# Performance work log

Hardware: AMD Instinct MI355X
Metric: run time of the kernel (lower is better)

Reference implementation:

```python
import jax, jax.numpy as jnp
import numpy as np

B, T, C = 4, 2048, 1024
H = 16
D = C // H  # 64


def setup_inputs() -> dict:
    key = jax.random.key(0)
    ks = jax.random.split(key, 5)
    scale = 0.02
    x = jax.random.normal(ks[0], (B, T, C), dtype=jnp.float32)
    # Linear weights stored in [in, out] layout (equivalent to torch W.T)
    W_qkv = jax.random.normal(ks[1], (C, 3 * C), dtype=jnp.float32) * scale
    b_qkv = jax.random.normal(ks[2], (3 * C,), dtype=jnp.float32) * scale
    W_out = jax.random.normal(ks[3], (C, C), dtype=jnp.float32) * scale
    b_out = jax.random.normal(ks[4], (C,), dtype=jnp.float32) * scale
    return {"x": x, "W_qkv": W_qkv, "b_qkv": b_qkv, "W_out": W_out, "b_out": b_out}


def reference(x, W_qkv, b_qkv, W_out, b_out):
    Bx, Tx, Cx = x.shape
    qkv = x @ W_qkv + b_qkv                      # [B,T,3C]
    qkv = qkv.reshape(Bx, Tx, 3, H, D)
    q = jnp.transpose(qkv[:, :, 0], (0, 2, 1, 3))  # [B,H,T,D]
    k = jnp.transpose(qkv[:, :, 1], (0, 2, 1, 3))
    v = jnp.transpose(qkv[:, :, 2], (0, 2, 1, 3))
    scores = jnp.einsum('bhqd,bhkd->bhqk', q, k) / jnp.sqrt(jnp.float32(D))
    causal = jnp.tril(jnp.ones((Tx, Tx), dtype=bool))  # keep lower triangle
    scores = jnp.where(causal, scores, jnp.float32(-jnp.inf))
    w = jax.nn.softmax(scores, axis=-1)           # dropout p=0.0 (eval)
    out = jnp.einsum('bhqk,bhkd->bhqd', w, v)     # [B,H,T,D]
    out = jnp.transpose(out, (0, 2, 1, 3)).reshape(Bx, Tx, Cx)
    return out @ W_out + b_out
```

## Files before the change

### kernel.cpp

```cpp
#include <hip/hip_runtime.h>

typedef _Float16 f16;
typedef _Float16 f16x4 __attribute__((ext_vector_type(4)));
typedef _Float16 f16x8 __attribute__((ext_vector_type(8)));
typedef float    f32x4 __attribute__((ext_vector_type(4)));

#define B_ 4
#define T_ 2048
#define C_ 1024
#define H_ 16
#define D_ 64

__device__ __forceinline__ void gload_lds16(const f16* g, f16* l) {
  __builtin_amdgcn_global_load_lds(
      (const __attribute__((address_space(1))) unsigned int*)g,
      (__attribute__((address_space(3))) unsigned int*)l, 16, 0, 0);
}

__global__ void cvt_kernel(const float* __restrict__ in, f16* __restrict__ out, int n4) {
  int i = blockIdx.x * blockDim.x + threadIdx.x;
  int stride = gridDim.x * blockDim.x;
  for (; i < n4; i += stride) {
    float4 v = ((const float4*)in)[i];
    f16x4 h = { (f16)v.x, (f16)v.y, (f16)v.z, (f16)v.w };
    ((f16x4*)out)[i] = h;
  }
}

__global__ void transpose_cvt_kernel(const float* __restrict__ W, f16* __restrict__ Wt,
                                     int K, int N) {
  __shared__ f16 tile[32][33];
  int bx = blockIdx.x, by = blockIdx.y;
  int tx = threadIdx.x & 31, ty = threadIdx.x >> 5;
  #pragma unroll
  for (int i = ty; i < 32; i += 8)
    tile[i][tx] = (f16)W[(size_t)(by * 32 + i) * N + bx * 32 + tx];
  __syncthreads();
  #pragma unroll
  for (int i = ty; i < 32; i += 8)
    Wt[(size_t)(bx * 32 + i) * K + by * 32 + tx] = tile[tx][i];
}

template <int EPI>
__global__ __launch_bounds__(256, 3)
void gemm_kernel(const f16* __restrict__ A, const f16* __restrict__ Bt,
                 const float* __restrict__ bias, float* __restrict__ outF,
                 f16* __restrict__ q, f16* __restrict__ kk, f16* __restrict__ vt,
                 int M, int N, int K) {
  __shared__ __align__(16) f16 As[3][128 * 32];
  __shared__ __align__(16) f16 Bs[3][128 * 32];
  const int nbn = N >> 7;
  const int bid = blockIdx.x;
  const int bm = bid / nbn, bn = bid % nbn;
  const int m0 = bm << 7, n0 = bn << 7;
  const int tid = threadIdx.x;
  const int lane = tid & 63, wid = tid >> 6;
  const int wr = wid >> 1, wc = wid & 1;

  f32x4 acc[4][4] = {};

  const int srow = lane >> 2;
  const int scol = (((lane & 3) ^ ((lane >> 2) & 3)) << 3);
  const f16* Abase = A + (size_t)(m0 + srow) * K + scol;
  const f16* Bbase = Bt + (size_t)(n0 + srow) * K + scol;

  auto stage = [&](int buf, int kt) {
    const int c0 = wid * 2;
    #pragma unroll
    for (int c = c0; c < c0 + 2; ++c) {
      gload_lds16(Abase + (size_t)c * 16 * K + kt * 32, &As[buf][c * 512]);
      gload_lds16(Bbase + (size_t)c * 16 * K + kt * 32, &Bs[buf][c * 512]);
    }
  };

  const int g = lane >> 4;
  const int rr = lane & 15;
  const int swz = (g ^ (rr & 3)) << 4;

  auto compute = [&](int buf) {
    f16x8 af[4], bf[4];
    #pragma unroll
    for (int t = 0; t < 4; ++t) {
      af[t] = *(const f16x8*)((const char*)&As[buf][0] + (wr * 64 + t * 16 + rr) * 64 + swz);
      bf[t] = *(const f16x8*)((const char*)&Bs[buf][0] + (wc * 64 + t * 16 + rr) * 64 + swz);
    }
    __builtin_amdgcn_s_setprio(1);
    #pragma unroll
    for (int i = 0; i < 4; ++i)
      #pragma unroll
      for (int j = 0; j < 4; ++j)
        acc[i][j] = __builtin_amdgcn_mfma_f32_16x16x32_f16(af[i], bf[j], acc[i][j], 0, 0, 0);
    __builtin_amdgcn_s_setprio(0);
  };

  const int nk = K >> 5;
  int bcur = 0, bnext = 1, bnn = 2;
  stage(0, 0);
  stage(1, 1);
  asm volatile("s_waitcnt vmcnt(4)" ::: "memory");
  __builtin_amdgcn_s_barrier();
  __builtin_amdgcn_sched_barrier(0);
  for (int t = 0; t < nk; ++t) {
    if (t + 2 < nk) stage(bnn, t + 2);
    compute(bcur);
    if (t + 1 < nk) {
      if (t + 2 < nk) asm volatile("s_waitcnt vmcnt(4)" ::: "memory");
      else            asm volatile("s_waitcnt vmcnt(0)" ::: "memory");
      __builtin_amdgcn_s_barrier();
      __builtin_amdgcn_sched_barrier(0);
    }
    const int tmp = bcur; bcur = bnext; bnext = bnn; bnn = tmp;
  }

  const int col = lane & 15;
  const int row4 = (lane >> 4) << 2;
  #pragma unroll
  for (int i = 0; i < 4; ++i) {
    #pragma unroll
    for (int j = 0; j < 4; ++j) {
      const int n = n0 + wc * 64 + j * 16 + col;
      const float bn_ = bias[n];
      #pragma unroll
      for (int r = 0; r < 4; ++r) {
        const int m = m0 + wr * 64 + i * 16 + row4 + r;
        const float v = acc[i][j][r] + bn_;
        if (EPI == 1) {
          outF[(size_t)m * N + n] = v;
        } else {
          const int which = n >> 10;
          const int cc = n & 1023;
          const int h = cc >> 6, d = cc & 63;
          const int b = m >> 11, t = m & 2047;
          const size_t bh = (size_t)b * 16 + h;
          const f16 hv = (f16)v;
          if (which == 0)      q [(bh * T_ + t) * D_ + d] = hv;
          else if (which == 1) kk[(bh * T_ + t) * D_ + d] = hv;
          else                 vt[(bh * D_ + d) * T_ + t] = hv;
        }
      }
    }
  }
}

__global__ __launch_bounds__(256, 2)
void attn_kernel(const f16* __restrict__ Q, const f16* __restrict__ Kg,
                 const f16* __restrict__ Vt, f16* __restrict__ Aout) {
  __shared__ __align__(16) f16 Ks[4][64 * 64];
  __shared__ __align__(16) f16 Vs[4][64 * 64];
  __shared__ __align__(16) f16 Pt[4][32 * 64];

  const int bid = blockIdx.x;
  const int wgid = (bid & 7) * 64 + (bid >> 3);
  const int bh = wgid >> 3;
  const int pr = wgid & 7;
  const int lane = threadIdx.x & 63, w = threadIdx.x >> 6;
  const int col = lane & 15;
  const int g = lane >> 4;
  const int ko = g << 3;

  const f16* Qp = Q + (size_t)bh * T_ * D_;
  const f16* Kp = Kg + (size_t)bh * T_ * D_;
  const f16* Vp = Vt + (size_t)bh * D_ * T_;

  const int sr = lane >> 3;
  const int sc = ((lane & 7) ^ (sr & 7)) << 3;

  auto stage = [&](int buf, int kb) {
    #pragma unroll
    for (int c2 = 0; c2 < 2; ++c2) {
      const int c = (w << 1) + c2;
      gload_lds16(Kp + (size_t)(kb + (c << 3) + sr) * D_ + sc, &Ks[buf][c * 512]);
      gload_lds16(Vp + (size_t)((c << 3) + sr) * T_ + kb + sc, &Vs[buf][c * 512]);
    }
  };
  auto ldsK = [&](int buf, int krow, int d0) -> f16x8 {
    const int off = krow * 128 + ((d0 << 1) ^ ((krow & 7) << 4));
    return *(const f16x8*)((const char*)&Ks[buf][0] + off);
  };
  auto ldsV = [&](int buf, int drow, int k0) -> f16x8 {
    const int off = drow * 128 + ((k0 << 1) ^ ((drow & 7) << 4));
    return *(const f16x8*)((const char*)&Vs[buf][0] + off);
  };

  char* PtW = (char*)&Pt[w][0];
  const int b = bh >> 4, hd = bh & 15;

  #pragma unroll 1
  for (int tt = 0; tt < 2; ++tt) {
    const int ti = tt ? (15 - pr) : pr;
    const int qrow0 = (ti << 7) + (w << 5);
    const int np = ti + 1;

    f16x8 qf[2][2];
    #pragma unroll
    for (int h = 0; h < 2; ++h)
      #pragma unroll
      for (int s = 0; s < 2; ++s) {
        f16x8 t = *(const f16x8*)&Qp[(size_t)(qrow0 + h * 16 + col) * D_ + s * 32 + ko];
        #pragma unroll
        for (int e = 0; e < 8; ++e) t[e] = t[e] * (f16)0.125f;
        qf[h][s] = t;
      }

    f32x4 o[2][4] = {};
    float m[2] = {-1e30f, -1e30f}, l[2] = {0.f, 0.f};

    auto COMPUTE = [&](int buf, int kb) {
      f32x4 sc2[2][4] = {};
      #pragma unroll
      for (int s = 0; s < 2; ++s)
        #pragma unroll
        for (int mt = 0; mt < 4; ++mt) {
          f16x8 kf = ldsK(buf, mt * 16 + col, s * 32 + ko);
          sc2[0][mt] = __builtin_amdgcn_mfma_f32_16x16x32_f16(kf, qf[0][s], sc2[0][mt], 0, 0, 0);
          sc2[1][mt] = __builtin_amdgcn_mfma_f32_16x16x32_f16(kf, qf[1][s], sc2[1][mt], 0, 0, 0);
        }

      if (kb + 63 > qrow0) {
        #pragma unroll
        for (int mt = 0; mt < 4; ++mt)
          #pragma unroll
          for (int r = 0; r < 4; ++r) {
            const int kv = kb + mt * 16 + (g << 2) + r;
            if (kv > qrow0 + col)      sc2[0][mt][r] = -1e30f;
            if (kv > qrow0 + 16 + col) sc2[1][mt][r] = -1e30f;
          }
      }

      float mx[2];
      #pragma unroll
      for (int h = 0; h < 2; ++h) {
        float v = fmaxf(fmaxf(fmaxf(sc2[h][0][0], sc2[h][0][1]), fmaxf(sc2[h][0][2], sc2[h][0][3])),
                        fmaxf(fmaxf(sc2[h][1][0], sc2[h][1][1]), fmaxf(sc2[h][1][2], sc2[h][1][3])));
        v = fmaxf(v, fmaxf(fmaxf(fmaxf(sc2[h][2][0], sc2[h][2][1]), fmaxf(sc2[h][2][2], sc2[h][2][3])),
                           fmaxf(fmaxf(sc2[h][3][0], sc2[h][3][1]), fmaxf(sc2[h][3][2], sc2[h][3][3]))));
        v = fmaxf(v, __shfl_xor(v, 16, 64));
        v = fmaxf(v, __shfl_xor(v, 32, 64));
        mx[h] = v;
      }

      if (!__all(fmaxf(mx[0] - m[0], mx[1] - m[1]) <= 8.f)) {
        #pragma unroll
        for (int h = 0; h < 2; ++h) {
          const float mnew = fmaxf(m[h], mx[h]);
          const float alpha = __expf(m[h] - mnew);
          m[h] = mnew;
          l[h] *= alpha;
          #pragma unroll
          for (int mt = 0; mt < 4; ++mt)
            #pragma unroll
            for (int r = 0; r < 4; ++r) o[h][mt][r] *= alpha;
        }
      }

      #pragma unroll
      for (int h = 0; h < 2; ++h) {
        float rs = 0.f;
        #pragma unroll
        for (int mt = 0; mt < 4; ++mt) {
          f16x4 ph;
          #pragma unroll
          for (int r = 0; r < 4; ++r) {
            const float p = __expf(sc2[h][mt][r] - m[h]);
            rs += p;
            ph[r] = (f16)p;
          }
          *(f16x4*)(PtW + (h * 16 + col) * 128 + (((mt << 5) + (g << 3)) ^ ((col & 7) << 4))) = ph;
        }
        rs += __shfl_xor(rs, 16, 64);
        rs += __shfl_xor(rs, 32, 64);
        l[h] += rs;
      }

      #pragma unroll
      for (int s = 0; s < 2; ++s) {
        const int pcb = ((s << 6) + (g << 4)) ^ ((col & 7) << 4);
        f16x8 pb0 = *(const f16x8*)(PtW + col * 128 + pcb);
        f16x8 pb1 = *(const f16x8*)(PtW + (16 + col) * 128 + pcb);
        #pragma unroll
        for (int mt = 0; mt < 4; ++mt) {
          f16x8 vf = ldsV(buf, mt * 16 + col, s * 32 + ko);
          o[0][mt] = __builtin_amdgcn_mfma_f32_16x16x32_f16(vf, pb0, o[0][mt], 0, 0, 0);
          o[1][mt] = __builtin_amdgcn_mfma_f32_16x16x32_f16(vf, pb1, o[1][mt], 0, 0, 0);
        }
      }
    };

    stage(0, 0);
    stage(1, 64);
    asm volatile("s_waitcnt vmcnt(0)" ::: "memory");
    __builtin_amdgcn_s_barrier();
    __builtin_amdgcn_sched_barrier(0);

    #pragma unroll 1
    for (int j = 0; j < np; ++j) {
      const int kb0 = j << 7;
      const int s0 = (j << 1) & 3, s1 = ((j << 1) + 1) & 3;
      if (j + 1 < np) {
        stage((s0 + 2) & 3, kb0 + 128);
        stage((s1 + 2) & 3, kb0 + 192);
      }
      COMPUTE(s0, kb0);
      if (kb0 + 64 <= qrow0 + 31) COMPUTE(s1, kb0 + 64);

      __builtin_amdgcn_sched_barrier(0);
      asm volatile("s_waitcnt vmcnt(0)" ::: "memory");
      __builtin_amdgcn_s_barrier();
      __builtin_amdgcn_sched_barrier(0);
    }

    #pragma unroll
    for (int h = 0; h < 2; ++h) {
      const float inv = 1.0f / l[h];
      const int t = qrow0 + h * 16 + col;
      const size_t rowoff = ((size_t)b * T_ + t) * C_ + (size_t)hd * D_;
      #pragma unroll
      for (int mt = 0; mt < 4; ++mt) {
        f16x4 ov;
        #pragma unroll
        for (int r = 0; r < 4; ++r) ov[r] = (f16)(o[h][mt][r] * inv);
        *(f16x4*)&Aout[rowoff + mt * 16 + (g << 2)] = ov;
      }
    }
    __builtin_amdgcn_s_barrier();
  }
}

extern "C" void kernel_launch(void* const* d_in, const int* in_sizes, int n_in,
                              void* d_out, int out_size, void* d_ws, size_t ws_size,
                              hipStream_t stream) {
  const float* x    = (const float*)d_in[0];
  const float* Wqkv = (const float*)d_in[1];
  const float* bqkv = (const float*)d_in[2];
  const float* Wout = (const float*)d_in[3];
  const float* bout = (const float*)d_in[4];
  float* out = (float*)d_out;

  char* ws = (char*)d_ws;
  f16* xb     = (f16*)ws;
  f16* Wqkv_t = (f16*)(ws + (16u << 20));
  f16* Wout_t = (f16*)(ws + (22u << 20));
  f16* Qb     = (f16*)(ws + (24u << 20));
  f16* Kb     = (f16*)(ws + (40u << 20));
  f16* Vtb    = (f16*)(ws + (56u << 20));

  cvt_kernel<<<2048, 256, 0, stream>>>(x, xb, (B_ * T_ * C_) / 4);
  dim3 g1(3072 / 32, 1024 / 32);
  transpose_cvt_kernel<<<g1, 256, 0, stream>>>(Wqkv, Wqkv_t, 1024, 3072);
  dim3 g2(1024 / 32, 1024 / 32);
  transpose_cvt_kernel<<<g2, 256, 0, stream>>>(Wout, Wout_t, 1024, 1024);

  gemm_kernel<0><<<64 * 24, 256, 0, stream>>>(xb, Wqkv_t, bqkv, nullptr,
                                              Qb, Kb, Vtb, 8192, 3072, 1024);
  attn_kernel<<<512, 256, 0, stream>>>(Qb, Kb, Vtb, xb );
  gemm_kernel<1><<<64 * 8, 256, 0, stream>>>(xb, Wout_t, bout, out,
                                             nullptr, nullptr, nullptr, 8192, 1024, 1024);
}
```

Baseline: 207.9 us.

## Use exp2 softmax, MFMA priority hints, and merge weight transpose launches

When the exp2 builtin is available, folds log2(e) into the query scale and uses the hardware exp2 instruction in the attention softmax, and scales the rescale threshold to match. It also raises wave priority around the two MFMA blocks with s_setprio so matrix work is issued ahead of other waves. Finally, the two weight transpose/convert launches are merged into a single kernel, saving one launch. The exp2 path slightly changes rounding of the f16 query scale, and the priority hints may or may not help scheduling.

Result: faster. 203.5 us (-2.1%).

```diff
diff --git a/kernel.cpp b/kernel.cpp
--- a/kernel.cpp
+++ b/kernel.cpp
@@ -10,6 +10,16 @@
 #define C_ 1024
 #define H_ 16
 #define D_ 64
+
+#if __has_builtin(__builtin_amdgcn_exp2f)
+#define FAST_EXP(x) __builtin_amdgcn_exp2f(x)
+#define QSCALE (0.125f * 1.44269504f)
+#define DTHR 11.54f
+#else
+#define FAST_EXP(x) __expf(x)
+#define QSCALE 0.125f
+#define DTHR 8.0f
+#endif
 
 __device__ __forceinline__ void gload_lds16(const f16* g, f16* l) {
   __builtin_amdgcn_global_load_lds(
@@ -27,10 +37,14 @@
   }
 }
 
-__global__ void transpose_cvt_kernel(const float* __restrict__ W, f16* __restrict__ Wt,
-                                     int K, int N) {
+__global__ void transpose2_kernel(const float* __restrict__ Wqkv, f16* __restrict__ WqkvT,
+                                  const float* __restrict__ Wout, f16* __restrict__ WoutT) {
   __shared__ f16 tile[32][33];
+  const int K = 1024;
   int bx = blockIdx.x, by = blockIdx.y;
+  const float* W; f16* Wt; int N;
+  if (bx < 96) { W = Wqkv; Wt = WqkvT; N = 3072; }
+  else         { W = Wout; Wt = WoutT; N = 1024; bx -= 96; }
   int tx = threadIdx.x & 31, ty = threadIdx.x >> 5;
   #pragma unroll
   for (int i = ty; i < 32; i += 8)
@@ -191,6 +205,7 @@
     const int qrow0 = (ti << 7) + (w << 5);
     const int np = ti + 1;
 
+    const f16 qsc = (f16)QSCALE;
     f16x8 qf[2][2];
     #pragma unroll
     for (int h = 0; h < 2; ++h)
@@ -198,7 +213,7 @@
       for (int s = 0; s < 2; ++s) {
         f16x8 t = *(const f16x8*)&Qp[(size_t)(qrow0 + h * 16 + col) * D_ + s * 32 + ko];
         #pragma unroll
-        for (int e = 0; e < 8; ++e) t[e] = t[e] * (f16)0.125f;
+        for (int e = 0; e < 8; ++e) t[e] = t[e] * qsc;
         qf[h][s] = t;
       }
 
@@ -207,6 +222,7 @@
 
     auto COMPUTE = [&](int buf, int kb) {
       f32x4 sc2[2][4] = {};
+      __builtin_amdgcn_s_setprio(1);
       #pragma unroll
       for (int s = 0; s < 2; ++s)
         #pragma unroll
@@ -215,6 +231,7 @@
           sc2[0][mt] = __builtin_amdgcn_mfma_f32_16x16x32_f16(kf, qf[0][s], sc2[0][mt], 0, 0, 0);
           sc2[1][mt] = __builtin_amdgcn_mfma_f32_16x16x32_f16(kf, qf[1][s], sc2[1][mt], 0, 0, 0);
         }
+      __builtin_amdgcn_s_setprio(0);
 
       if (kb + 63 > qrow0) {
         #pragma unroll
@@ -239,11 +256,11 @@
         mx[h] = v;
       }
 
-      if (!__all(fmaxf(mx[0] - m[0], mx[1] - m[1]) <= 8.f)) {
+      if (!__all(fmaxf(mx[0] - m[0], mx[1] - m[1]) <= DTHR)) {
         #pragma unroll
         for (int h = 0; h < 2; ++h) {
           const float mnew = fmaxf(m[h], mx[h]);
-          const float alpha = __expf(m[h] - mnew);
+          const float alpha = FAST_EXP(m[h] - mnew);
           m[h] = mnew;
           l[h] *= alpha;
           #pragma unroll
@@ -261,7 +278,7 @@
           f16x4 ph;
           #pragma unroll
           for (int r = 0; r < 4; ++r) {
-            const float p = __expf(sc2[h][mt][r] - m[h]);
+            const float p = FAST_EXP(sc2[h][mt][r] - m[h]);
             rs += p;
             ph[r] = (f16)p;
           }
@@ -272,6 +289,7 @@
         l[h] += rs;
       }
 
+      __builtin_amdgcn_s_setprio(1);
       #pragma unroll
       for (int s = 0; s < 2; ++s) {
         const int pcb = ((s << 6) + (g << 4)) ^ ((col & 7) << 4);
@@ -284,6 +302,7 @@
           o[1][mt] = __builtin_amdgcn_mfma_f32_16x16x32_f16(vf, pb1, o[1][mt], 0, 0, 0);
         }
       }
+      __builtin_amdgcn_s_setprio(0);
     };
 
     stage(0, 0);
@@ -345,10 +364,8 @@
   f16* Vtb    = (f16*)(ws + (56u << 20));
 
   cvt_kernel<<<2048, 256, 0, stream>>>(x, xb, (B_ * T_ * C_) / 4);
-  dim3 g1(3072 / 32, 1024 / 32);
-  transpose_cvt_kernel<<<g1, 256, 0, stream>>>(Wqkv, Wqkv_t, 1024, 3072);
-  dim3 g2(1024 / 32, 1024 / 32);
-  transpose_cvt_kernel<<<g2, 256, 0, stream>>>(Wout, Wout_t, 1024, 1024);
+  dim3 gt(128, 32);
+  transpose2_kernel<<<gt, 256, 0, stream>>>(Wqkv, Wqkv_t, Wout, Wout_t);
 
   gemm_kernel<0><<<64 * 24, 256, 0, stream>>>(xb, Wqkv_t, bqkv, nullptr,
                                               Qb, Kb, Vtb, 8192, 3072, 1024);
```
